# Performance work log

Hardware: AMD Instinct MI355X
Metric: run time of the kernel (lower is better)

Reference implementation:

```python
import jax, jax.numpy as jnp
import numpy as np

N, D, C = 8192, 256, 100
MARGIN = 1.0


def setup_inputs() -> dict:
    key = jax.random.key(0)
    k1, k2 = jax.random.split(key)
    features = jax.random.normal(k1, (N, D), dtype=jnp.float32)
    labels = jax.random.randint(k2, (N,), 0, C, dtype=jnp.int64)
    return {"features": features, "labels": labels}


def _pairwise_dist(f):
    # f: [N, D] L2-normalized rows. Euclidean distance matrix [N, N].
    sq = jnp.sum(f * f, axis=1)  # [N]
    d2 = sq[:, None] + sq[None, :] - 2.0 * (f @ f.T)
    d2 = jnp.maximum(d2, 0.0)
    # safe sqrt: zero distance (incl. diagonal) -> 0 with finite grad
    pos = d2 > 0.0
    return jnp.where(pos, jnp.sqrt(jnp.where(pos, d2, 1.0)), 0.0)


def reference(features, labels):
    # F.normalize(p=2, dim=1)
    norm = jnp.linalg.norm(features, axis=1, keepdims=True)
    f = features / jnp.maximum(norm, 1e-12)

    dist = _pairwise_dist(f)  # [N, N]

    onehot = jax.nn.one_hot(labels, C, dtype=f.dtype)  # [N, C]
    counts = jnp.sum(onehot, axis=0)  # [C]
    # S[a, b] = sum_{i in a, j in b} dist[i, j]
    S = onehot.T @ dist @ onehot  # [C, C]

    # intra: per-class mean over off-diagonal pairs (diag of dist is 0),
    # only classes with count > 1, then mean over those classes
    intra_valid = counts > 1.0
    intra_denom = jnp.where(intra_valid, counts * (counts - 1.0), 1.0)
    intra_per_class = jnp.diag(S) / intra_denom
    n_intra = jnp.sum(intra_valid.astype(f.dtype))
    intra = jnp.where(
        n_intra > 0,
        jnp.sum(jnp.where(intra_valid, intra_per_class, 0.0)) / jnp.maximum(n_intra, 1.0),
        0.0,
    )

    # inter: per class-pair (a < b, both present) mean distance, then mean over pairs
    pair_cnt = counts[:, None] * counts[None, :]
    inter_mat = S / jnp.where(pair_cnt > 0.0, pair_cnt, 1.0)
    present = counts > 0.0
    upper = jnp.triu(jnp.ones((C, C), dtype=bool), k=1)
    pair_mask = upper & present[:, None] & present[None, :]
    n_pairs = jnp.sum(pair_mask.astype(f.dtype))
    inter = jnp.where(
        n_pairs > 0,
        jnp.sum(jnp.where(pair_mask, inter_mat, 0.0)) / jnp.maximum(n_pairs, 1.0),
        1.0,
    )

    loss = jax.nn.relu(intra - inter + MARGIN)
    return loss  # scalar; .mean() of a scalar is itself
```

## Files before the change

kernel.cpp:

```cpp
#include <hip/hip_runtime.h>
#include <math.h>

#define N_ROWS 8192
#define D_DIM  256
#define C_CLS  100
#define BM 128
#define BK 128
#define NSTRIP (N_ROWS / BM)
#define NBLK (NSTRIP * (NSTRIP + 1) / 2)
#define UPK (C_CLS * (C_CLS + 1) / 2)
#define MAXSEG 4

typedef __attribute__((ext_vector_type(4))) float floatx4;

__device__ __forceinline__ void gl2lds16(const void* g, void* l) {
    __builtin_amdgcn_global_load_lds(
        (const __attribute__((address_space(1))) void*)g,
        (__attribute__((address_space(3))) void*)l, 16, 0, 0);
}

__global__ __launch_bounds__(256)
void prep_k(const float* __restrict__ in, const int* __restrict__ labels,
            unsigned int* __restrict__ fnb8, int* __restrict__ slab,
            int* __restrict__ offs, int* __restrict__ perm,
            float* __restrict__ Ug, int* __restrict__ ctr) {
    if (blockIdx.x == 0) {
        __shared__ int h[C_CLS];
        __shared__ int incl[128];
        __shared__ int oS[C_CLS + 1];
        __shared__ int cur[C_CLS];
        const int t = threadIdx.x;
        if (t < C_CLS) h[t] = 0;
        __syncthreads();
        int myl[32];
#pragma unroll
        for (int u = 0; u < 32; ++u) myl[u] = labels[t + u * 256];
#pragma unroll
        for (int u = 0; u < 32; ++u) atomicAdd(&h[myl[u]], 1);
        __syncthreads();
        if (t < 128) {
            const int lane = t & 63;
            int v = (t < C_CLS) ? h[t] : 0;
#pragma unroll
            for (int o = 1; o < 64; o <<= 1) {
                const int n = __shfl_up(v, o, 64);
                if (lane >= o) v += n;
            }
            incl[t] = v;
        }
        __syncthreads();
        if (t <= C_CLS)
            oS[t] = (t == 0) ? 0 : incl[t - 1] + ((t - 1) >= 64 ? incl[63] : 0);
        __syncthreads();
        if (t < C_CLS) cur[t] = oS[t];
        __syncthreads();
#pragma unroll
        for (int u = 0; u < 32; ++u) {
            const int i = t + u * 256;
            const int pos = atomicAdd(&cur[myl[u]], 1);
            slab[pos] = myl[u];
            perm[pos] = i;
        }
        if (t < C_CLS + 1) offs[t] = oS[t];
        for (int e = t; e < UPK; e += 256) Ug[e] = 0.f;
        if (t == 0) *ctr = 0;
    } else {
        const int row  = (blockIdx.x - 1) * 4 + (threadIdx.x >> 6);
        const int lane = threadIdx.x & 63;
        float4 v = ((const float4*)in)[row * 64 + lane];
        float s = v.x * v.x + v.y * v.y + v.z * v.z + v.w * v.w;
#pragma unroll
        for (int o = 32; o > 0; o >>= 1) s += __shfl_xor(s, o, 64);
        const float inv = 1.f / fmaxf(sqrtf(s), 1e-12f);
        int pk = __builtin_amdgcn_cvt_pk_fp8_f32(v.x * inv, v.y * inv, 0, 0);
        pk     = __builtin_amdgcn_cvt_pk_fp8_f32(v.z * inv, v.w * inv, pk, 1);
        fnb8[row * 64 + lane] = (unsigned int)pk;
    }
}

__global__ __launch_bounds__(256, 4)
void main_k(const unsigned char* __restrict__ fnb8, const int* __restrict__ slab,
            const int* __restrict__ offs_g, const int* __restrict__ perm,
            float* __restrict__ Ug, int* __restrict__ ctr,
            float* __restrict__ out) {
    __shared__ __align__(16) unsigned char As[BM * BK];
    __shared__ __align__(16) unsigned char Bs[BM * BK];
    __shared__ float red[4][MAXSEG * MAXSEG][17];
    __shared__ int soffs[C_CLS + 1];
    __shared__ int meta[4][4];
    __shared__ int flagS;

    const int t = threadIdx.x;

    int b = blockIdx.x, ti = 0, len = NSTRIP;
    while (b >= len) { b -= len; ++ti; --len; }
    const int tj = ti + b;
    const int i0 = ti * BM, j0 = tj * BM;

    if (t < C_CLS + 1) soffs[t] = offs_g[t];

    const int lane = t & 63;
    const int w    = t >> 6;
    const int m0 = (w & 1) * 64, n0 = (w >> 1) * 64;
    const int lr = lane & 15, lq = lane >> 4;
    const int swz = (lr >> 1) & 7;

    int abase[4], bbase[4];
#pragma unroll
    for (int mb = 0; mb < 4; ++mb) abase[mb] = (m0 + mb * 16 + lr) * BK;
#pragma unroll
    for (int nb = 0; nb < 4; ++nb) bbase[nb] = (n0 + nb * 16 + lr) * BK;

    int srow[4], skc[4], pA[4], pB[4];
#pragma unroll
    for (int u = 0; u < 4; ++u) {
        const int s = t + 256 * u;
        srow[u] = s >> 3;
        skc[u]  = (s & 7) ^ ((srow[u] >> 1) & 7);
    }
#pragma unroll
    for (int u = 0; u < 4; ++u) pA[u] = perm[i0 + srow[u]];
#pragma unroll
    for (int u = 0; u < 4; ++u) pB[u] = perm[j0 + srow[u]];

    floatx4 acc[4][4];
#pragma unroll
    for (int mb = 0; mb < 4; ++mb)
#pragma unroll
        for (int nb = 0; nb < 4; ++nb) acc[mb][nb] = 0.f;

#pragma unroll
    for (int k0 = 0; k0 < D_DIM; k0 += BK) {
        __syncthreads();
#pragma unroll
        for (int u = 0; u < 4; ++u)
            gl2lds16(&fnb8[((size_t)pA[u] << 8) + k0 + skc[u] * 16],
                     &As[(t + 256 * u) * 16]);
#pragma unroll
        for (int u = 0; u < 4; ++u)
            gl2lds16(&fnb8[((size_t)pB[u] << 8) + k0 + skc[u] * 16],
                     &Bs[(t + 256 * u) * 16]);
        __syncthreads();

#pragma unroll
        for (int si = 0; si < 4; ++si) {
            const int coff = ((((si * 2) + (lq >> 1)) ^ swz) << 4) + ((lq & 1) << 3);
            long a[4], bb[4];
#pragma unroll
            for (int mb = 0; mb < 4; ++mb) a[mb]  = *(const long*)&As[abase[mb] + coff];
#pragma unroll
            for (int nb = 0; nb < 4; ++nb) bb[nb] = *(const long*)&Bs[bbase[nb] + coff];
#pragma unroll
            for (int mb = 0; mb < 4; ++mb)
#pragma unroll
                for (int nb = 0; nb < 4; ++nb)
                    acc[mb][nb] = __builtin_amdgcn_mfma_f32_16x16x32_fp8_fp8(
                        a[mb], bb[nb], acc[mb][nb], 0, 0, 0);
        }
    }

    const bool diag = (ti == tj);
#pragma unroll
    for (int mb = 0; mb < 4; ++mb)
#pragma unroll
        for (int nb = 0; nb < 4; ++nb)
#pragma unroll
            for (int r = 0; r < 4; ++r) {
                const float g = acc[mb][nb][r];
                float dv = __builtin_amdgcn_sqrtf(fmaxf(2.f - 2.f * g, 0.f));
                const int rt = m0 + mb * 16 + lq * 4 + r;
                const int ct = n0 + nb * 16 + lr;
                if (diag && rt == ct) dv = 0.f;
                acc[mb][nb][r] = dv;
            }

    const int cA0 = __builtin_amdgcn_readfirstlane(slab[i0 + m0]);
    const int cA1 = __builtin_amdgcn_readfirstlane(slab[i0 + m0 + 63]);
    const int cB0 = __builtin_amdgcn_readfirstlane(slab[j0 + n0]);
    const int cB1 = __builtin_amdgcn_readfirstlane(slab[j0 + n0 + 63]);
    const int segsA = cA1 - cA0 + 1, segsB = cB1 - cB0 + 1;
    if (lane == 0) {
        meta[w][0] = cA0; meta[w][1] = cB0; meta[w][2] = segsA; meta[w][3] = segsB;
    }
    const float wscale = diag ? 1.f : 2.f;

    float rem[4][4];
#pragma unroll
    for (int mb = 0; mb < 4; ++mb)
#pragma unroll
        for (int r = 0; r < 4; ++r)
            rem[mb][r] = acc[mb][0][r] + acc[mb][1][r] + acc[mb][2][r] + acc[mb][3][r];

    for (int sb = 0; sb < segsB; ++sb) {
        const int cb = cB0 + sb;
        float colsum[4][4];
        if (sb == segsB - 1) {
#pragma unroll
            for (int mb = 0; mb < 4; ++mb)
#pragma unroll
                for (int r = 0; r < 4; ++r) colsum[mb][r] = rem[mb][r];
        } else {
            const int rb0 = max(soffs[cb]     - j0, n0);
            const int rb1 = min(soffs[cb + 1] - j0, n0 + 64);
#pragma unroll
            for (int mb = 0; mb < 4; ++mb)
#pragma unroll
                for (int r = 0; r < 4; ++r) colsum[mb][r] = 0.f;
#pragma unroll
            for (int nb = 0; nb < 4; ++nb) {
                const int ct = n0 + nb * 16 + lr;
                const float mk = ((ct >= rb0) & (ct < rb1)) ? 1.f : 0.f;
#pragma unroll
                for (int mb = 0; mb < 4; ++mb)
#pragma unroll
                    for (int r = 0; r < 4; ++r)
                        colsum[mb][r] = fmaf(mk, acc[mb][nb][r], colsum[mb][r]);
            }
#pragma unroll
            for (int mb = 0; mb < 4; ++mb)
#pragma unroll
                for (int r = 0; r < 4; ++r) rem[mb][r] -= colsum[mb][r];
        }
        for (int sa = 0; sa < segsA; ++sa) {
            const int ca = cA0 + sa;
            const int ra0 = max(soffs[ca]     - i0, m0);
            const int ra1 = min(soffs[ca + 1] - i0, m0 + 64);
            float v = 0.f;
#pragma unroll
            for (int mb = 0; mb < 4; ++mb) {
                const int rtb = m0 + mb * 16 + lq * 4;
#pragma unroll
                for (int r = 0; r < 4; ++r) {
                    const int rt = rtb + r;
                    const bool ir = (rt >= ra0) & (rt < ra1);
                    v += ir ? colsum[mb][r] : 0.f;
                }
            }
            if (sa < MAXSEG && sb < MAXSEG) {
                v += __shfl_xor(v, 1, 64);
                v += __shfl_xor(v, 2, 64);
                if ((lane & 3) == 0) red[w][sb * MAXSEG + sa][lane >> 2] = v;
            } else {
#pragma unroll
                for (int o = 32; o > 0; o >>= 1) v += __shfl_xor(v, o, 64);
                if (lane == 0 && v != 0.f) {
                    const int mn = min(ca, cb), mx = max(ca, cb);
                    atomicAdd(&Ug[mx + ((mn * (2 * C_CLS - 1 - mn)) >> 1)], wscale * v);
                }
            }
        }
    }

    __syncthreads();
    {
        const int combo = t >> 2, q = t & 3;
        const int wv = combo >> 4, sl = combo & 15;
        float s = red[wv][sl][q * 4 + 0] + red[wv][sl][q * 4 + 1]
                + red[wv][sl][q * 4 + 2] + red[wv][sl][q * 4 + 3];
        s += __shfl_xor(s, 1, 64);
        s += __shfl_xor(s, 2, 64);
        const int sa = sl & (MAXSEG - 1), sb = sl >> 2;
        if (q == 0 && sa < meta[wv][2] && sb < meta[wv][3] && s != 0.f) {
            const int ca = meta[wv][0] + sa, cb = meta[wv][1] + sb;
            const int mn = min(ca, cb), mx = max(ca, cb);
            atomicAdd(&Ug[mx + ((mn * (2 * C_CLS - 1 - mn)) >> 1)], wscale * s);
        }
    }

    __syncthreads();
    if (t == 0) {
        asm volatile("s_waitcnt vmcnt(0)" ::: "memory");
        flagS = (atomicAdd(ctr, 1) == NBLK - 1) ? 1 : 0;
    }
    __syncthreads();
    if (flagS) {
        float* const rf = (float*)&red[0][0][0];
        int*   const ri = (int*)&red[2][0][0];
        __threadfence();
        float s_intra = 0.f; int n_intra = 0;
        if (t < C_CLS) {
            const int c = soffs[t + 1] - soffs[t];
            if (c > 1) {
                const int idx = t + ((t * (2 * C_CLS - 1 - t)) >> 1);
                s_intra = Ug[idx] / ((float)c * (float)(c - 1));
                n_intra = 1;
            }
        }
        float s_inter = 0.f; int n_pairs = 0;
        for (int p = t; p < C_CLS * C_CLS; p += 256) {
            const int a = p / C_CLS, b2 = p - a * C_CLS;
            if (b2 > a) {
                const int ca = soffs[a + 1] - soffs[a];
                const int cb = soffs[b2 + 1] - soffs[b2];
                if (ca > 0 && cb > 0) {
                    const int idx = b2 + ((a * (2 * C_CLS - 1 - a)) >> 1);
                    s_inter += 0.5f * Ug[idx] / ((float)ca * (float)cb);
                    ++n_pairs;
                }
            }
        }
        rf[t] = s_intra; ri[t] = n_intra; __syncthreads();
        for (int s2 = 128; s2 > 0; s2 >>= 1) {
            if (t < s2) { rf[t] += rf[t + s2]; ri[t] += ri[t + s2]; }
            __syncthreads();
        }
        const float intra_sum = rf[0]; const int intra_n = ri[0];
        __syncthreads();
        rf[t] = s_inter; ri[t] = n_pairs; __syncthreads();
        for (int s2 = 128; s2 > 0; s2 >>= 1) {
            if (t < s2) { rf[t] += rf[t + s2]; ri[t] += ri[t + s2]; }
            __syncthreads();
        }
        if (t == 0) {
            const float inter_sum = rf[0]; const int pairs_n = ri[0];
            const float intra = (intra_n > 0) ? intra_sum / (float)intra_n : 0.f;
            const float inter = (pairs_n > 0) ? inter_sum / (float)pairs_n : 1.f;
            out[0] = fmaxf(intra - inter + 1.0f, 0.f);
        }
    }
}

extern "C" void kernel_launch(void* const* d_in, const int* in_sizes, int n_in,
                              void* d_out, int out_size, void* d_ws, size_t ws_size,
                              hipStream_t stream) {
    const float* feats  = (const float*)d_in[0];
    const int*   labels = (const int*)d_in[1];
    float* out = (float*)d_out;

    char* p = (char*)d_ws;
    unsigned char* fnb8 = (unsigned char*)p;  p += (size_t)N_ROWS * D_DIM;
    int*   slab = (int*)p;  p += (size_t)N_ROWS * sizeof(int);
    int*   perm = (int*)p;  p += (size_t)N_ROWS * sizeof(int);
    int*   offs = (int*)p;  p += 128 * sizeof(int);
    float* Ug   = (float*)p;  p += ((UPK + 31) / 32) * 32 * sizeof(float);
    int*   ctr  = (int*)p;

    prep_k <<<1 + N_ROWS / 4, 256, 0, stream>>>(feats, labels, (unsigned int*)fnb8,
                                                slab, offs, perm, Ug, ctr);
    main_k <<<NBLK, 256, 0, stream>>>(fnb8, slab, offs, perm, Ug, ctr, out);
}
```

Before: 117.7 us.

## Scatter normalized rows into class-sorted order before the GEMM

The fused prep kernel is split into a single-block label sort, run with 1024 threads, and a normalize kernel. The sort emits each row's destination index, and the normalize kernel writes every fp8 row straight to its sorted position. The main kernel then loads contiguous rows instead of gathering through a permutation array, which removes the perm loads and the indirect addressing. In exchange it adds a kernel launch and serializes the sort ahead of normalization, where before the two ran in parallel blocks.

```diff
diff --git a/kernel.cpp b/kernel.cpp
--- a/kernel.cpp
+++ b/kernel.cpp
@@ -19,70 +19,69 @@
         (__attribute__((address_space(3))) void*)l, 16, 0, 0);
 }
 
-__global__ __launch_bounds__(256)
-void prep_k(const float* __restrict__ in, const int* __restrict__ labels,
-            unsigned int* __restrict__ fnb8, int* __restrict__ slab,
-            int* __restrict__ offs, int* __restrict__ perm,
-            float* __restrict__ Ug, int* __restrict__ ctr) {
-    if (blockIdx.x == 0) {
-        __shared__ int h[C_CLS];
-        __shared__ int incl[128];
-        __shared__ int oS[C_CLS + 1];
-        __shared__ int cur[C_CLS];
-        const int t = threadIdx.x;
-        if (t < C_CLS) h[t] = 0;
-        __syncthreads();
-        int myl[32];
-#pragma unroll
-        for (int u = 0; u < 32; ++u) myl[u] = labels[t + u * 256];
-#pragma unroll
-        for (int u = 0; u < 32; ++u) atomicAdd(&h[myl[u]], 1);
-        __syncthreads();
-        if (t < 128) {
-            const int lane = t & 63;
-            int v = (t < C_CLS) ? h[t] : 0;
-#pragma unroll
-            for (int o = 1; o < 64; o <<= 1) {
-                const int n = __shfl_up(v, o, 64);
-                if (lane >= o) v += n;
-            }
-            incl[t] = v;
-        }
-        __syncthreads();
-        if (t <= C_CLS)
-            oS[t] = (t == 0) ? 0 : incl[t - 1] + ((t - 1) >= 64 ? incl[63] : 0);
-        __syncthreads();
-        if (t < C_CLS) cur[t] = oS[t];
-        __syncthreads();
-#pragma unroll
-        for (int u = 0; u < 32; ++u) {
-            const int i = t + u * 256;
-            const int pos = atomicAdd(&cur[myl[u]], 1);
-            slab[pos] = myl[u];
-            perm[pos] = i;
-        }
-        if (t < C_CLS + 1) offs[t] = oS[t];
-        for (int e = t; e < UPK; e += 256) Ug[e] = 0.f;
-        if (t == 0) *ctr = 0;
-    } else {
-        const int row  = (blockIdx.x - 1) * 4 + (threadIdx.x >> 6);
-        const int lane = threadIdx.x & 63;
-        float4 v = ((const float4*)in)[row * 64 + lane];
-        float s = v.x * v.x + v.y * v.y + v.z * v.z + v.w * v.w;
-#pragma unroll
-        for (int o = 32; o > 0; o >>= 1) s += __shfl_xor(s, o, 64);
-        const float inv = 1.f / fmaxf(sqrtf(s), 1e-12f);
-        int pk = __builtin_amdgcn_cvt_pk_fp8_f32(v.x * inv, v.y * inv, 0, 0);
-        pk     = __builtin_amdgcn_cvt_pk_fp8_f32(v.z * inv, v.w * inv, pk, 1);
-        fnb8[row * 64 + lane] = (unsigned int)pk;
-    }
+__global__ void sort_k(const int* __restrict__ labels, int* __restrict__ dest,
+                       int* __restrict__ slab, int* __restrict__ offs,
+                       float* __restrict__ Ug, int* __restrict__ ctr) {
+    __shared__ int h[C_CLS];
+    __shared__ int incl[128];
+    __shared__ int oS[C_CLS + 1];
+    __shared__ int cur[C_CLS];
+    const int t = threadIdx.x;
+    if (t < C_CLS) h[t] = 0;
+    __syncthreads();
+    int myl[8];
+#pragma unroll
+    for (int u = 0; u < 8; ++u) myl[u] = labels[t + u * 1024];
+#pragma unroll
+    for (int u = 0; u < 8; ++u) atomicAdd(&h[myl[u]], 1);
+    __syncthreads();
+    if (t < 128) {
+        const int lane = t & 63;
+        int v = (t < C_CLS) ? h[t] : 0;
+#pragma unroll
+        for (int o = 1; o < 64; o <<= 1) {
+            const int n = __shfl_up(v, o, 64);
+            if (lane >= o) v += n;
+        }
+        incl[t] = v;
+    }
+    __syncthreads();
+    if (t <= C_CLS)
+        oS[t] = (t == 0) ? 0 : incl[t - 1] + ((t - 1) >= 64 ? incl[63] : 0);
+    __syncthreads();
+    if (t < C_CLS) cur[t] = oS[t];
+    __syncthreads();
+#pragma unroll
+    for (int u = 0; u < 8; ++u) {
+        const int i = t + u * 1024;
+        const int pos = atomicAdd(&cur[myl[u]], 1);
+        dest[i] = pos;
+        slab[pos] = myl[u];
+    }
+    if (t < C_CLS + 1) offs[t] = oS[t];
+    for (int e = t; e < UPK; e += 1024) Ug[e] = 0.f;
+    if (t == 0) *ctr = 0;
+}
+
+__global__ void normalize_k(const float* __restrict__ in, const int* __restrict__ dest,
+                            unsigned int* __restrict__ fnb8) {
+    const int row  = blockIdx.x * 4 + (threadIdx.x >> 6);
+    const int lane = threadIdx.x & 63;
+    float4 v = ((const float4*)in)[row * 64 + lane];
+    float s = v.x * v.x + v.y * v.y + v.z * v.z + v.w * v.w;
+#pragma unroll
+    for (int o = 32; o > 0; o >>= 1) s += __shfl_xor(s, o, 64);
+    const float inv = 1.f / fmaxf(sqrtf(s), 1e-12f);
+    const int d = dest[row];
+    int pk = __builtin_amdgcn_cvt_pk_fp8_f32(v.x * inv, v.y * inv, 0, 0);
+    pk     = __builtin_amdgcn_cvt_pk_fp8_f32(v.z * inv, v.w * inv, pk, 1);
+    fnb8[d * 64 + lane] = (unsigned int)pk;
 }
 
 __global__ __launch_bounds__(256, 4)
 void main_k(const unsigned char* __restrict__ fnb8, const int* __restrict__ slab,
-            const int* __restrict__ offs_g, const int* __restrict__ perm,
-            float* __restrict__ Ug, int* __restrict__ ctr,
-            float* __restrict__ out) {
+            const int* __restrict__ offs_g, float* __restrict__ Ug,
+            int* __restrict__ ctr, float* __restrict__ out) {
     __shared__ __align__(16) unsigned char As[BM * BK];
     __shared__ __align__(16) unsigned char Bs[BM * BK];
     __shared__ float red[4][MAXSEG * MAXSEG][17];
@@ -111,17 +110,13 @@
 #pragma unroll
     for (int nb = 0; nb < 4; ++nb) bbase[nb] = (n0 + nb * 16 + lr) * BK;
 
-    int srow[4], skc[4], pA[4], pB[4];
+    int srow[4], skc[4];
 #pragma unroll
     for (int u = 0; u < 4; ++u) {
         const int s = t + 256 * u;
         srow[u] = s >> 3;
         skc[u]  = (s & 7) ^ ((srow[u] >> 1) & 7);
     }
-#pragma unroll
-    for (int u = 0; u < 4; ++u) pA[u] = perm[i0 + srow[u]];
-#pragma unroll
-    for (int u = 0; u < 4; ++u) pB[u] = perm[j0 + srow[u]];
 
     floatx4 acc[4][4];
 #pragma unroll
@@ -134,11 +129,11 @@
         __syncthreads();
 #pragma unroll
         for (int u = 0; u < 4; ++u)
-            gl2lds16(&fnb8[((size_t)pA[u] << 8) + k0 + skc[u] * 16],
+            gl2lds16(&fnb8[(size_t)(i0 + srow[u]) * D_DIM + k0 + skc[u] * 16],
                      &As[(t + 256 * u) * 16]);
 #pragma unroll
         for (int u = 0; u < 4; ++u)
-            gl2lds16(&fnb8[((size_t)pB[u] << 8) + k0 + skc[u] * 16],
+            gl2lds16(&fnb8[(size_t)(j0 + srow[u]) * D_DIM + k0 + skc[u] * 16],
                      &Bs[(t + 256 * u) * 16]);
         __syncthreads();
 
@@ -330,12 +325,12 @@
     char* p = (char*)d_ws;
     unsigned char* fnb8 = (unsigned char*)p;  p += (size_t)N_ROWS * D_DIM;
     int*   slab = (int*)p;  p += (size_t)N_ROWS * sizeof(int);
-    int*   perm = (int*)p;  p += (size_t)N_ROWS * sizeof(int);
+    int*   dest = (int*)p;  p += (size_t)N_ROWS * sizeof(int);
     int*   offs = (int*)p;  p += 128 * sizeof(int);
     float* Ug   = (float*)p;  p += ((UPK + 31) / 32) * 32 * sizeof(float);
     int*   ctr  = (int*)p;
 
-    prep_k <<<1 + N_ROWS / 4, 256, 0, stream>>>(feats, labels, (unsigned int*)fnb8,
-                                                slab, offs, perm, Ug, ctr);
-    main_k <<<NBLK, 256, 0, stream>>>(fnb8, slab, offs, perm, Ug, ctr, out);
-}
+    sort_k     <<<1, 1024, 0, stream>>>(labels, dest, slab, offs, Ug, ctr);
+    normalize_k<<<N_ROWS / 4, 256, 0, stream>>>(feats, dest, (unsigned int*)fnb8);
+    main_k     <<<NBLK, 256, 0, stream>>>(fnb8, slab, offs, Ug, ctr, out);
+}
```

New measurement: 117.7 us. About the same (-0.1%).
